# Performance work log

Hardware: AMD Instinct MI355X
Metric: run time of the kernel (lower is better)

The kernel has to match this reference:

```python
import jax, jax.numpy as jnp
import numpy as np

EMBD = 512
HEADS = 8
HEAD = EMBD // HEADS


def setup_inputs() -> dict:
    key = jax.random.key(0)
    ks = jax.random.split(key, 9)
    B, M = 4, 2048
    s = 1.0 / np.sqrt(EMBD)
    inp = {
        "x": jax.random.normal(ks[0], (B, M, EMBD), dtype=jnp.float32),
        "wq": jax.random.uniform(ks[1], (EMBD, EMBD), jnp.float32, -s, s),
        "bq": jnp.zeros((EMBD,), jnp.float32),
        "wk": jax.random.uniform(ks[2], (EMBD, EMBD), jnp.float32, -s, s),
        "bk": jnp.zeros((EMBD,), jnp.float32),
        "wv": jax.random.uniform(ks[3], (EMBD, EMBD), jnp.float32, -s, s),
        "bv": jnp.zeros((EMBD,), jnp.float32),
        "wo": jax.random.uniform(ks[4], (EMBD, EMBD), jnp.float32, -s, s),
        "bo": jnp.zeros((EMBD,), jnp.float32),
        "gamma": jnp.ones((EMBD,), jnp.float32),
        "beta": jnp.zeros((EMBD,), jnp.float32),
    }
    return inp


def layer_norm(x, gamma, beta, eps=1e-5):
    mu = jnp.mean(x, axis=-1, keepdims=True)
    var = jnp.mean(jnp.square(x - mu), axis=-1, keepdims=True)
    return (x - mu) * jax.lax.rsqrt(var + eps) * gamma + beta


def reference(x, wq, bq, wk, bk, wv, bv, wo, bo, gamma, beta):
    B, M, _ = x.shape
    norm = layer_norm(x, gamma, beta)
    # projections; reshape to [B, H, M, Dh]
    def proj(w, b):
        return (norm @ w.T + b).reshape(B, M, HEADS, HEAD).transpose(0, 2, 1, 3)
    q = proj(wq, bq)
    k = proj(wk, bk)
    v = proj(wv, bv)
    scores = jnp.einsum("bhmd,bhnd->bhmn", q, k) / np.sqrt(HEAD)
    # exclude self-attention on the diagonal
    diag = jnp.eye(M, dtype=bool)
    scores = jnp.where(diag, -jnp.inf, scores)
    attn = jax.nn.softmax(scores, axis=-1)
    ctx = jnp.einsum("bhmn,bhnd->bhmd", attn, v)
    ctx = ctx.transpose(0, 2, 1, 3).reshape(B, M, EMBD)
    out = ctx @ wo.T + bo
    return (out + x, attn)
```

## Files before the change

### kernel.cpp

```cpp
#include <hip/hip_runtime.h>

#define B_   4
#define H_   8
#define M_   2048
#define D_   512
#define DH_  64

typedef short  bf16x8 __attribute__((ext_vector_type(8)));
typedef short  bf16x4 __attribute__((ext_vector_type(4)));
typedef float  f32x4  __attribute__((ext_vector_type(4)));
typedef unsigned short u16x4 __attribute__((ext_vector_type(4)));
typedef unsigned int   u32x2 __attribute__((ext_vector_type(2)));

#define EXPC 0.18033688011112042f

static __device__ __forceinline__ unsigned short f2bf(float f) {
  unsigned u = __float_as_uint(f);
  u += 0x7fffu + ((u >> 16) & 1u);
  return (unsigned short)(u >> 16);
}

static __device__ __forceinline__ unsigned cvtpk(float lo, float hi) {
  unsigned r;
  asm("v_cvt_pk_bf16_f32 %0, %1, %2" : "=v"(r) : "v"(lo), "v"(hi));
  return r;
}

static __device__ __forceinline__ f32x4 mfma16(bf16x4 a, bf16x4 b, f32x4 c) {
  asm("v_mfma_f32_16x16x16_bf16 %0, %1, %2, %0" : "+v"(c) : "v"(a), "v"(b));
  return c;
}

static __device__ __forceinline__ int swz128(int row, int byteoff) {
  return row * 128 + (byteoff ^ ((row & 7) << 4));
}

static __device__ __forceinline__ void glds16(const void* g, void* l) {
  __builtin_amdgcn_global_load_lds(
      (const __attribute__((address_space(1))) unsigned*)g,
      (__attribute__((address_space(3))) unsigned*)l, 16, 0, 0);
}

static __device__ __forceinline__ void stage_tile(
    const char* g0, size_t rstride, char* lds, int t) {
  const int r0 = t >> 3, c0 = t & 7;
  const char* src = g0 + (size_t)r0 * rstride + ((c0 ^ (r0 & 7)) << 4);
  char* dst = lds + ((t & 192) << 4);
  #pragma unroll
  for (int c = 0; c < 4; ++c)
    glds16(src + (size_t)c * 32 * rstride, dst + c * 4096);
}

__global__ __launch_bounds__(256) void ln_kernel(
    const float* __restrict__ x, const float* __restrict__ gamma,
    const float* __restrict__ beta, unsigned short* __restrict__ xn)
{
  int row = blockIdx.x;
  int t = threadIdx.x;
  const float* xr = x + (size_t)row * D_;
  float v0 = xr[t], v1 = xr[t + 256];
  float s = v0 + v1, ss = v0 * v0 + v1 * v1;
  #pragma unroll
  for (int m = 1; m < 64; m <<= 1) {
    s  += __shfl_xor(s, m);
    ss += __shfl_xor(ss, m);
  }
  __shared__ float red[8];
  int wid = t >> 6;
  if ((t & 63) == 0) { red[wid] = s; red[wid + 4] = ss; }
  __syncthreads();
  s  = red[0] + red[1] + red[2] + red[3];
  ss = red[4] + red[5] + red[6] + red[7];
  float mu  = s * (1.0f / D_);
  float var = ss * (1.0f / D_) - mu * mu;
  float rstd = rsqrtf(var + 1e-5f);
  unsigned short* o = xn + (size_t)row * D_;
  o[t]       = f2bf((v0 - mu) * rstd * gamma[t]       + beta[t]);
  o[t + 256] = f2bf((v1 - mu) * rstd * gamma[t + 256] + beta[t + 256]);
}

__global__ __launch_bounds__(256) void cast_w_kernel(
    const float* __restrict__ wq, const float* __restrict__ wk,
    const float* __restrict__ wv, const float* __restrict__ wo,
    unsigned short* __restrict__ wqkv, unsigned short* __restrict__ wob)
{
  int i = blockIdx.x * 256 + threadIdx.x;
  wqkv[i]          = f2bf(wq[i]);
  wqkv[i + 262144] = f2bf(wk[i]);
  wqkv[i + 524288] = f2bf(wv[i]);
  wob[i]           = f2bf(wo[i]);
}

__global__ __launch_bounds__(256) void qkv_gemm(
    const unsigned short* __restrict__ xn,
    const unsigned short* __restrict__ wqkv,
    const float* __restrict__ bq, const float* __restrict__ bk,
    const float* __restrict__ bv,
    unsigned short* __restrict__ q, unsigned short* __restrict__ Kp,
    unsigned short* __restrict__ Vp)
{
  __shared__ __align__(16) char As[128 * 128];
  __shared__ __align__(16) char Bs[128 * 128];
  const int m0 = blockIdx.x * 128;
  const int n0 = blockIdx.y * 128;
  const int t = threadIdx.x, wid = t >> 6, lane = t & 63;
  const int wr = (wid >> 1) * 64, wc = (wid & 1) * 64;
  const int cl = lane & 15, rg = lane >> 4;
  const f32x4 z4 = {0.f, 0.f, 0.f, 0.f};
  const bool isv = (n0 >= 1024);

  const char* agb = (const char*)xn   + (size_t)m0 * 1024;
  const char* bgb = (const char*)wqkv + (size_t)n0 * 1024;

  f32x4 acc[4][4];
  #pragma unroll
  for (int i = 0; i < 4; ++i)
    #pragma unroll
    for (int j = 0; j < 4; ++j) acc[i][j] = z4;

  for (int k0 = 0; k0 < 512; k0 += 64) {
    __syncthreads();
    stage_tile(agb + k0 * 2, 1024, As, t);
    stage_tile(bgb + k0 * 2, 1024, Bs, t);
    __syncthreads();
    #pragma unroll
    for (int ks = 0; ks < 2; ++ks) {
      int koff = ks * 64 + rg * 16;
      bf16x8 af[4], bfr[4];
      #pragma unroll
      for (int i = 0; i < 4; ++i)
        af[i] = *(const bf16x8*)(As + swz128(wr + i * 16 + cl, koff));
      #pragma unroll
      for (int j = 0; j < 4; ++j)
        bfr[j] = *(const bf16x8*)(Bs + swz128(wc + j * 16 + cl, koff));
      if (isv) {
        #pragma unroll
        for (int i = 0; i < 4; ++i)
          #pragma unroll
          for (int j = 0; j < 4; ++j)
            acc[i][j] = __builtin_amdgcn_mfma_f32_16x16x32_bf16(af[i], bfr[j], acc[i][j], 0, 0, 0);
      } else {
        #pragma unroll
        for (int j = 0; j < 4; ++j)
          #pragma unroll
          for (int i = 0; i < 4; ++i)
            acc[j][i] = __builtin_amdgcn_mfma_f32_16x16x32_bf16(bfr[j], af[i], acc[j][i], 0, 0, 0);
      }
    }
  }

  if (isv) {
    #pragma unroll
    for (int j = 0; j < 4; ++j) {
      int n = n0 + wc + j * 16 + cl;
      int nn = n & 511;
      int h = nn >> 6, dh = nn & 63;
      int jd = dh >> 4, cld = dh & 15;
      float bias = bv[nn];
      #pragma unroll
      for (int i = 0; i < 4; ++i) {
        int mrow = m0 + wr + i * 16 + rg * 4;
        int b = mrow >> 11, mm = mrow & 2047;
        int nt = mm >> 6, nl = mm & 63;
        int jp = nl >> 5, half = (nl >> 4) & 1, rgv = (nl >> 2) & 3;
        u32x2 u;
        u[0] = cvtpk(acc[i][j][0] + bias, acc[i][j][1] + bias);
        u[1] = cvtpk(acc[i][j][2] + bias, acc[i][j][3] + bias);
        size_t off = ((((size_t)(b * H_ + h) * 32 + nt) * 4 + jd) * 2 + jp) * 512
                   + (rgv * 16 + cld) * 8 + half * 4;
        *(u16x4*)(Vp + off) = __builtin_bit_cast(u16x4, u);
      }
    }
  } else {
    const int mat = n0 >> 9;
    #pragma unroll
    for (int j = 0; j < 4; ++j) {
      int nn0 = ((n0 + wc) & 511) + j * 16 + rg * 4;
      int h = nn0 >> 6, dh = nn0 & 63;
      f32x4 b4 = *(const f32x4*)((mat ? bk : bq) + nn0);
      #pragma unroll
      for (int i = 0; i < 4; ++i) {
        int mrow = m0 + wr + i * 16 + cl;
        int b = mrow >> 11, mm = mrow & 2047;
        u32x2 u;
        u[0] = cvtpk(acc[j][i][0] + b4[0], acc[j][i][1] + b4[1]);
        u[1] = cvtpk(acc[j][i][2] + b4[2], acc[j][i][3] + b4[3]);
        if (mat == 0) {
          *(u16x4*)(q + ((size_t)(b * H_ + h) * M_ + mm) * DH_ + dh) =
              __builtin_bit_cast(u16x4, u);
        } else {
          int ks = dh >> 5, rgk = (dh >> 3) & 3, e0 = dh & 7;
          size_t off = ((((size_t)(b * H_ + h) * 32 + (mm >> 6)) * 4 + ((mm >> 4) & 3)) * 2 + ks) * 512
                     + (rgk * 16 + (mm & 15)) * 8 + e0;
          *(u16x4*)(Kp + off) = __builtin_bit_cast(u16x4, u);
        }
      }
    }
  }
}

__global__ __launch_bounds__(256, 4) void attn_kernel(
    const unsigned short* __restrict__ q,
    const unsigned short* __restrict__ Kp,
    const unsigned short* __restrict__ Vp,
    float* __restrict__ attn,
    unsigned short* __restrict__ ctx)
{
  __shared__ __align__(16) char Ps[4][2048];

  const int flat = blockIdx.x;
  const int bh = (flat & 7) * 4 + ((flat >> 3) >> 5);
  const int mb = (flat >> 3) & 31;
  const int m0 = mb * 64;
  const int t = threadIdx.x, wid = t >> 6, lane = t & 63;
  const int wr = wid * 16, cl = lane & 15, rg = lane >> 4;
  const int m_g = m0 + wr + cl;
  const f32x4 z4 = {0.f, 0.f, 0.f, 0.f};

  const char* qb = (const char*)(q + (size_t)bh * M_ * DH_);
  const unsigned short* kpb = Kp + (size_t)bh * 131072;
  const unsigned short* vpb = Vp + (size_t)bh * 131072;
  float* ab = attn + (size_t)bh * M_ * M_;

  bf16x8 qf[2];
  #pragma unroll
  for (int ks = 0; ks < 2; ++ks)
    qf[ks] = *(const bf16x8*)(qb + (size_t)m_g * 128 + ks * 64 + rg * 16);

  float psum = 0.f;
  for (int nt = 0; nt < 32; ++nt) {
    const unsigned short* kch = kpb + (size_t)nt * 4096;
    f32x4 s[4];
    #pragma unroll
    for (int j = 0; j < 4; ++j) s[j] = z4;
    #pragma unroll
    for (int ks = 0; ks < 2; ++ks)
      #pragma unroll
      for (int j = 0; j < 4; ++j) {
        bf16x8 kf = *(const bf16x8*)(kch + (j * 2 + ks) * 512 + lane * 8);
        s[j] = __builtin_amdgcn_mfma_f32_16x16x32_bf16(kf, qf[ks], s[j], 0, 0, 0);
      }
    if (nt == mb) {
      #pragma unroll
      for (int j = 0; j < 4; ++j)
        #pragma unroll
        for (int r = 0; r < 4; ++r) {
          int n_g = nt * 64 + j * 16 + rg * 4 + r;
          float p = __builtin_amdgcn_exp2f(s[j][r] * EXPC);
          psum += (n_g == m_g) ? 0.f : p;
        }
    } else {
      #pragma unroll
      for (int j = 0; j < 4; ++j)
        #pragma unroll
        for (int r = 0; r < 4; ++r)
          psum += __builtin_amdgcn_exp2f(s[j][r] * EXPC);
    }
  }
  psum += __shfl_xor(psum, 16);
  psum += __shfl_xor(psum, 32);
  const float rv = 1.0f / psum;

  f32x4 oc[4];
  #pragma unroll
  for (int j = 0; j < 4; ++j) oc[j] = z4;

  const int srow = lane >> 4;
  const int sch  = lane & 15;

  asm volatile("s_nop 7" :::);

  for (int nt = 0; nt < 32; ++nt) {
    const unsigned short* kch = kpb + (size_t)nt * 4096;
    const unsigned short* vch = vpb + (size_t)nt * 4096;
    f32x4 s[4];
    #pragma unroll
    for (int j = 0; j < 4; ++j) s[j] = z4;
    #pragma unroll
    for (int ks = 0; ks < 2; ++ks)
      #pragma unroll
      for (int j = 0; j < 4; ++j) {
        bf16x8 kf = *(const bf16x8*)(kch + (j * 2 + ks) * 512 + lane * 8);
        s[j] = __builtin_amdgcn_mfma_f32_16x16x32_bf16(kf, qf[ks], s[j], 0, 0, 0);
      }
    const bool dtile = (nt == mb);
    bf16x4 pb[4];
    #pragma unroll
    for (int j = 0; j < 4; ++j) {
      f32x4 pv;
      #pragma unroll
      for (int r = 0; r < 4; ++r) {
        int n_g = nt * 64 + j * 16 + rg * 4 + r;
        float p = __builtin_amdgcn_exp2f(s[j][r] * EXPC) * rv;
        pv[r] = (dtile && n_g == m_g) ? 0.f : p;
      }
      u32x2 u;
      u[0] = cvtpk(pv[0], pv[1]);
      u[1] = cvtpk(pv[2], pv[3]);
      pb[j] = __builtin_bit_cast(bf16x4, u);
      *(u32x2*)(Ps[wid] + swz128(cl, j * 32 + rg * 8)) = u;
    }
    {
      float* abase = ab + ((size_t)(m0 + wr + srow)) * M_ + nt * 64 + sch * 4;
      #pragma unroll
      for (int it = 0; it < 4; ++it) {
        u16x4 pu = *(const u16x4*)(Ps[wid] + swz128(it * 4 + srow, sch * 8));
        f32x4 pv;
        #pragma unroll
        for (int r = 0; r < 4; ++r) pv[r] = __uint_as_float((unsigned)pu[r] << 16);
        __builtin_nontemporal_store(pv, (f32x4*)(abase + (size_t)it * 4 * M_));
      }
    }
    #pragma unroll
    for (int jp = 0; jp < 2; ++jp)
      #pragma unroll
      for (int jd = 0; jd < 4; ++jd) {
        bf16x8 w = *(const bf16x8*)(vch + (jd * 2 + jp) * 512 + lane * 8);
        bf16x4 vlo = __builtin_shufflevector(w, w, 0, 1, 2, 3);
        bf16x4 vhi = __builtin_shufflevector(w, w, 4, 5, 6, 7);
        oc[jd] = mfma16(vlo, pb[jp * 2],     oc[jd]);
        oc[jd] = mfma16(vhi, pb[jp * 2 + 1], oc[jd]);
      }
  }

  asm volatile("s_nop 7\n\ts_nop 7" :::);

  int b = bh >> 3, h = bh & 7;
  unsigned short* crow = ctx + ((size_t)b * M_ + m_g) * D_ + h * DH_ + rg * 4;
  #pragma unroll
  for (int jd = 0; jd < 4; ++jd) {
    u32x2 u;
    u[0] = cvtpk(oc[jd][0], oc[jd][1]);
    u[1] = cvtpk(oc[jd][2], oc[jd][3]);
    *(u32x2*)(crow + jd * 16) = u;
  }
}

__global__ __launch_bounds__(256) void out_gemm(
    const unsigned short* __restrict__ ctxb,
    const unsigned short* __restrict__ wob,
    const float* __restrict__ bo,
    const float* __restrict__ x,
    float* __restrict__ out)
{
  __shared__ __align__(16) char As[128 * 128];
  __shared__ __align__(16) char Bs[128 * 128];
  const int m0 = blockIdx.x * 128;
  const int n0 = blockIdx.y * 128;
  const int t = threadIdx.x, wid = t >> 6, lane = t & 63;
  const int wr = (wid >> 1) * 64, wc = (wid & 1) * 64;
  const int cl = lane & 15, rg = lane >> 4;
  const f32x4 z4 = {0.f, 0.f, 0.f, 0.f};

  const char* agb = (const char*)ctxb + (size_t)m0 * 1024;
  const char* bgb = (const char*)wob  + (size_t)n0 * 1024;

  f32x4 acc[4][4];
  #pragma unroll
  for (int j = 0; j < 4; ++j)
    #pragma unroll
    for (int i = 0; i < 4; ++i) acc[j][i] = z4;

  for (int k0 = 0; k0 < 512; k0 += 64) {
    __syncthreads();
    stage_tile(agb + k0 * 2, 1024, As, t);
    stage_tile(bgb + k0 * 2, 1024, Bs, t);
    __syncthreads();
    #pragma unroll
    for (int ks = 0; ks < 2; ++ks) {
      int koff = ks * 64 + rg * 16;
      bf16x8 af[4], bfr[4];
      #pragma unroll
      for (int i = 0; i < 4; ++i)
        af[i] = *(const bf16x8*)(As + swz128(wr + i * 16 + cl, koff));
      #pragma unroll
      for (int j = 0; j < 4; ++j)
        bfr[j] = *(const bf16x8*)(Bs + swz128(wc + j * 16 + cl, koff));
      #pragma unroll
      for (int j = 0; j < 4; ++j)
        #pragma unroll
        for (int i = 0; i < 4; ++i)
          acc[j][i] = __builtin_amdgcn_mfma_f32_16x16x32_bf16(bfr[j], af[i], acc[j][i], 0, 0, 0);
    }
  }

  #pragma unroll
  for (int j = 0; j < 4; ++j) {
    int nb = n0 + wc + j * 16 + rg * 4;
    f32x4 bo4 = *(const f32x4*)(bo + nb);
    #pragma unroll
    for (int i = 0; i < 4; ++i) {
      int m = m0 + wr + i * 16 + cl;
      f32x4 x4 = *(const f32x4*)(x + (size_t)m * 512 + nb);
      f32x4 o;
      #pragma unroll
      for (int r = 0; r < 4; ++r) o[r] = acc[j][i][r] + bo4[r] + x4[r];
      *(f32x4*)(out + (size_t)m * 512 + nb) = o;
    }
  }
}

extern "C" void kernel_launch(void* const* d_in, const int* in_sizes, int n_in,
                              void* d_out, int out_size, void* d_ws, size_t ws_size,
                              hipStream_t stream) {
  const float* x     = (const float*)d_in[0];
  const float* wq    = (const float*)d_in[1];
  const float* bq    = (const float*)d_in[2];
  const float* wk    = (const float*)d_in[3];
  const float* bk    = (const float*)d_in[4];
  const float* wv    = (const float*)d_in[5];
  const float* bv    = (const float*)d_in[6];
  const float* wo    = (const float*)d_in[7];
  const float* bo    = (const float*)d_in[8];
  const float* gamma = (const float*)d_in[9];
  const float* beta  = (const float*)d_in[10];

  char* ws = (char*)d_ws;
  unsigned short* xn   = (unsigned short*)(ws);
  unsigned short* wqkv = (unsigned short*)(ws + 8388608);
  unsigned short* wob  = (unsigned short*)(ws + 9961472);
  unsigned short* qb   = (unsigned short*)(ws + 10485760);
  unsigned short* Kp   = (unsigned short*)(ws + 18874368);
  unsigned short* Vp   = (unsigned short*)(ws + 27262976);
  unsigned short* ctx  = (unsigned short*)(ws + 35651584);

  float* out  = (float*)d_out;
  float* attn = (float*)d_out + 4194304;

  ln_kernel<<<8192, 256, 0, stream>>>(x, gamma, beta, xn);
  cast_w_kernel<<<1024, 256, 0, stream>>>(wq, wk, wv, wo, wqkv, wob);
  qkv_gemm<<<dim3(64, 12), 256, 0, stream>>>(xn, wqkv, bq, bk, bv, qb, Kp, Vp);
  attn_kernel<<<1024, 256, 0, stream>>>(qb, Kp, Vp, attn, ctx);
  out_gemm<<<dim3(64, 4), 256, 0, stream>>>(ctx, wob, bo, x, out);
}
```

Measured before the change: 201.6 us.

## Process two query tiles per attention block and halve out-GEMM N tile

Each attention block now handles 128 query rows as two 64-row halves. The first half's output pass is fused with the second half's row-sum pass, so each K tile loaded from memory serves both halves. This cuts the number of K sweeps per query row from two to one and a half, at the cost of more registers and lower occupancy (launch bounds 2). The output GEMM switches to 128x64 tiles, doubling its grid to 512 blocks to fill more CUs.

```diff
diff --git a/kernel.cpp b/kernel.cpp
--- a/kernel.cpp
+++ b/kernel.cpp
@@ -49,6 +49,17 @@
   #pragma unroll
   for (int c = 0; c < 4; ++c)
     glds16(src + (size_t)c * 32 * rstride, dst + c * 4096);
+}
+
+static __device__ __forceinline__ void stage64(
+    const char* g0, size_t rstride, char* lds, int t) {
+  #pragma unroll
+  for (int c = 0; c < 2; ++c) {
+    int s = c * 256 + t;
+    int row = s >> 3, ch = s & 7;
+    const char* src = g0 + (size_t)row * rstride + ((ch ^ (row & 7)) << 4);
+    glds16(src, lds + c * 4096 + ((t & 192) << 4));
+  }
 }
 
 __global__ __launch_bounds__(256) void ln_kernel(
@@ -199,7 +210,7 @@
   }
 }
 
-__global__ __launch_bounds__(256, 4) void attn_kernel(
+__global__ __launch_bounds__(256, 2) void attn_kernel(
     const unsigned short* __restrict__ q,
     const unsigned short* __restrict__ Kp,
     const unsigned short* __restrict__ Vp,
@@ -209,12 +220,14 @@
   __shared__ __align__(16) char Ps[4][2048];
 
   const int flat = blockIdx.x;
-  const int bh = (flat & 7) * 4 + ((flat >> 3) >> 5);
-  const int mb = (flat >> 3) & 31;
-  const int m0 = mb * 64;
+  const int bh = (flat & 7) * 4 + ((flat >> 3) >> 4);
+  const int u  = (flat >> 3) & 15;
+  const int m0 = u * 128;
+  const int ntA = u * 2, ntB = u * 2 + 1;
   const int t = threadIdx.x, wid = t >> 6, lane = t & 63;
   const int wr = wid * 16, cl = lane & 15, rg = lane >> 4;
-  const int m_g = m0 + wr + cl;
+  const int mA = m0 + wr + cl;
+  const int mB = mA + 64;
   const f32x4 z4 = {0.f, 0.f, 0.f, 0.f};
 
   const char* qb = (const char*)(q + (size_t)bh * M_ * DH_);
@@ -222,12 +235,17 @@
   const unsigned short* vpb = Vp + (size_t)bh * 131072;
   float* ab = attn + (size_t)bh * M_ * M_;
 
-  bf16x8 qf[2];
-  #pragma unroll
-  for (int ks = 0; ks < 2; ++ks)
-    qf[ks] = *(const bf16x8*)(qb + (size_t)m_g * 128 + ks * 64 + rg * 16);
-
-  float psum = 0.f;
+  bf16x8 qfA[2], qfB[2];
+  #pragma unroll
+  for (int ks = 0; ks < 2; ++ks) {
+    qfA[ks] = *(const bf16x8*)(qb + (size_t)mA * 128 + ks * 64 + rg * 16);
+    qfB[ks] = *(const bf16x8*)(qb + (size_t)mB * 128 + ks * 64 + rg * 16);
+  }
+
+  const int srow = lane >> 4;
+  const int sch  = lane & 15;
+
+  float psumA = 0.f;
   for (int nt = 0; nt < 32; ++nt) {
     const unsigned short* kch = kpb + (size_t)nt * 4096;
     f32x4 s[4];
@@ -238,36 +256,136 @@
       #pragma unroll
       for (int j = 0; j < 4; ++j) {
         bf16x8 kf = *(const bf16x8*)(kch + (j * 2 + ks) * 512 + lane * 8);
-        s[j] = __builtin_amdgcn_mfma_f32_16x16x32_bf16(kf, qf[ks], s[j], 0, 0, 0);
-      }
-    if (nt == mb) {
+        s[j] = __builtin_amdgcn_mfma_f32_16x16x32_bf16(kf, qfA[ks], s[j], 0, 0, 0);
+      }
+    if (nt == ntA) {
       #pragma unroll
       for (int j = 0; j < 4; ++j)
         #pragma unroll
         for (int r = 0; r < 4; ++r) {
           int n_g = nt * 64 + j * 16 + rg * 4 + r;
           float p = __builtin_amdgcn_exp2f(s[j][r] * EXPC);
-          psum += (n_g == m_g) ? 0.f : p;
+          psumA += (n_g == mA) ? 0.f : p;
         }
     } else {
       #pragma unroll
       for (int j = 0; j < 4; ++j)
         #pragma unroll
         for (int r = 0; r < 4; ++r)
-          psum += __builtin_amdgcn_exp2f(s[j][r] * EXPC);
-    }
-  }
-  psum += __shfl_xor(psum, 16);
-  psum += __shfl_xor(psum, 32);
-  const float rv = 1.0f / psum;
-
-  f32x4 oc[4];
-  #pragma unroll
-  for (int j = 0; j < 4; ++j) oc[j] = z4;
-
-  const int srow = lane >> 4;
-  const int sch  = lane & 15;
-
+          psumA += __builtin_amdgcn_exp2f(s[j][r] * EXPC);
+    }
+  }
+  psumA += __shfl_xor(psumA, 16);
+  psumA += __shfl_xor(psumA, 32);
+  const float rvA = 1.0f / psumA;
+
+  asm volatile("s_nop 7" :::);
+
+  f32x4 ocA[4];
+  #pragma unroll
+  for (int j = 0; j < 4; ++j) ocA[j] = z4;
+  float psumB = 0.f;
+
+  for (int nt = 0; nt < 32; ++nt) {
+    const unsigned short* kch = kpb + (size_t)nt * 4096;
+    const unsigned short* vch = vpb + (size_t)nt * 4096;
+    bf16x8 kf[8], vf[8];
+    #pragma unroll
+    for (int jk = 0; jk < 8; ++jk)
+      kf[jk] = *(const bf16x8*)(kch + jk * 512 + lane * 8);
+    #pragma unroll
+    for (int jk = 0; jk < 8; ++jk)
+      vf[jk] = *(const bf16x8*)(vch + jk * 512 + lane * 8);
+    f32x4 s[4];
+    #pragma unroll
+    for (int j = 0; j < 4; ++j) s[j] = z4;
+    #pragma unroll
+    for (int ks = 0; ks < 2; ++ks)
+      #pragma unroll
+      for (int j = 0; j < 4; ++j)
+        s[j] = __builtin_amdgcn_mfma_f32_16x16x32_bf16(kf[j * 2 + ks], qfA[ks], s[j], 0, 0, 0);
+    const bool dA = (nt == ntA);
+    bf16x4 pb[4];
+    #pragma unroll
+    for (int j = 0; j < 4; ++j) {
+      f32x4 pv;
+      #pragma unroll
+      for (int r = 0; r < 4; ++r) {
+        int n_g = nt * 64 + j * 16 + rg * 4 + r;
+        float p = __builtin_amdgcn_exp2f(s[j][r] * EXPC) * rvA;
+        pv[r] = (dA && n_g == mA) ? 0.f : p;
+      }
+      u32x2 uu;
+      uu[0] = cvtpk(pv[0], pv[1]);
+      uu[1] = cvtpk(pv[2], pv[3]);
+      pb[j] = __builtin_bit_cast(bf16x4, uu);
+      *(u32x2*)(Ps[wid] + swz128(cl, j * 32 + rg * 8)) = uu;
+    }
+    {
+      float* abase = ab + ((size_t)(m0 + wr + srow)) * M_ + nt * 64 + sch * 4;
+      #pragma unroll
+      for (int it = 0; it < 4; ++it) {
+        u16x4 pu = *(const u16x4*)(Ps[wid] + swz128(it * 4 + srow, sch * 8));
+        f32x4 pv;
+        #pragma unroll
+        for (int r = 0; r < 4; ++r) pv[r] = __uint_as_float((unsigned)pu[r] << 16);
+        __builtin_nontemporal_store(pv, (f32x4*)(abase + (size_t)it * 4 * M_));
+      }
+    }
+    #pragma unroll
+    for (int jp = 0; jp < 2; ++jp)
+      #pragma unroll
+      for (int jd = 0; jd < 4; ++jd) {
+        bf16x8 w = vf[jd * 2 + jp];
+        bf16x4 vlo = __builtin_shufflevector(w, w, 0, 1, 2, 3);
+        bf16x4 vhi = __builtin_shufflevector(w, w, 4, 5, 6, 7);
+        ocA[jd] = mfma16(vlo, pb[jp * 2],     ocA[jd]);
+        ocA[jd] = mfma16(vhi, pb[jp * 2 + 1], ocA[jd]);
+      }
+    #pragma unroll
+    for (int j = 0; j < 4; ++j) s[j] = z4;
+    #pragma unroll
+    for (int ks = 0; ks < 2; ++ks)
+      #pragma unroll
+      for (int j = 0; j < 4; ++j)
+        s[j] = __builtin_amdgcn_mfma_f32_16x16x32_bf16(kf[j * 2 + ks], qfB[ks], s[j], 0, 0, 0);
+    if (nt == ntB) {
+      #pragma unroll
+      for (int j = 0; j < 4; ++j)
+        #pragma unroll
+        for (int r = 0; r < 4; ++r) {
+          int n_g = nt * 64 + j * 16 + rg * 4 + r;
+          float p = __builtin_amdgcn_exp2f(s[j][r] * EXPC);
+          psumB += (n_g == mB) ? 0.f : p;
+        }
+    } else {
+      #pragma unroll
+      for (int j = 0; j < 4; ++j)
+        #pragma unroll
+        for (int r = 0; r < 4; ++r)
+          psumB += __builtin_amdgcn_exp2f(s[j][r] * EXPC);
+    }
+  }
+  psumB += __shfl_xor(psumB, 16);
+  psumB += __shfl_xor(psumB, 32);
+  const float rvB = 1.0f / psumB;
+
+  {
+    int b = bh >> 3, h = bh & 7;
+    asm volatile("s_nop 7\n\ts_nop 7" :::);
+    unsigned short* crow = ctx + ((size_t)b * M_ + mA) * D_ + h * DH_ + rg * 4;
+    #pragma unroll
+    for (int jd = 0; jd < 4; ++jd) {
+      u32x2 uu;
+      uu[0] = cvtpk(ocA[jd][0], ocA[jd][1]);
+      uu[1] = cvtpk(ocA[jd][2], ocA[jd][3]);
+      *(u32x2*)(crow + jd * 16) = uu;
+    }
+  }
+
+  f32x4 ocB[4];
+  #pragma unroll
+  for (int j = 0; j < 4; ++j) ocB[j] = z4;
   asm volatile("s_nop 7" :::);
 
   for (int nt = 0; nt < 32; ++nt) {
@@ -281,9 +399,9 @@
       #pragma unroll
       for (int j = 0; j < 4; ++j) {
         bf16x8 kf = *(const bf16x8*)(kch + (j * 2 + ks) * 512 + lane * 8);
-        s[j] = __builtin_amdgcn_mfma_f32_16x16x32_bf16(kf, qf[ks], s[j], 0, 0, 0);
-      }
-    const bool dtile = (nt == mb);
+        s[j] = __builtin_amdgcn_mfma_f32_16x16x32_bf16(kf, qfB[ks], s[j], 0, 0, 0);
+      }
+    const bool dB = (nt == ntB);
     bf16x4 pb[4];
     #pragma unroll
     for (int j = 0; j < 4; ++j) {
@@ -291,17 +409,17 @@
       #pragma unroll
       for (int r = 0; r < 4; ++r) {
         int n_g = nt * 64 + j * 16 + rg * 4 + r;
-        float p = __builtin_amdgcn_exp2f(s[j][r] * EXPC) * rv;
-        pv[r] = (dtile && n_g == m_g) ? 0.f : p;
-      }
-      u32x2 u;
-      u[0] = cvtpk(pv[0], pv[1]);
-      u[1] = cvtpk(pv[2], pv[3]);
-      pb[j] = __builtin_bit_cast(bf16x4, u);
-      *(u32x2*)(Ps[wid] + swz128(cl, j * 32 + rg * 8)) = u;
+        float p = __builtin_amdgcn_exp2f(s[j][r] * EXPC) * rvB;
+        pv[r] = (dB && n_g == mB) ? 0.f : p;
+      }
+      u32x2 uu;
+      uu[0] = cvtpk(pv[0], pv[1]);
+      uu[1] = cvtpk(pv[2], pv[3]);
+      pb[j] = __builtin_bit_cast(bf16x4, uu);
+      *(u32x2*)(Ps[wid] + swz128(cl, j * 32 + rg * 8)) = uu;
     }
     {
-      float* abase = ab + ((size_t)(m0 + wr + srow)) * M_ + nt * 64 + sch * 4;
+      float* abase = ab + ((size_t)(m0 + 64 + wr + srow)) * M_ + nt * 64 + sch * 4;
       #pragma unroll
       for (int it = 0; it < 4; ++it) {
         u16x4 pu = *(const u16x4*)(Ps[wid] + swz128(it * 4 + srow, sch * 8));
@@ -318,21 +436,23 @@
         bf16x8 w = *(const bf16x8*)(vch + (jd * 2 + jp) * 512 + lane * 8);
         bf16x4 vlo = __builtin_shufflevector(w, w, 0, 1, 2, 3);
         bf16x4 vhi = __builtin_shufflevector(w, w, 4, 5, 6, 7);
-        oc[jd] = mfma16(vlo, pb[jp * 2],     oc[jd]);
-        oc[jd] = mfma16(vhi, pb[jp * 2 + 1], oc[jd]);
+        ocB[jd] = mfma16(vlo, pb[jp * 2],     ocB[jd]);
+        ocB[jd] = mfma16(vhi, pb[jp * 2 + 1], ocB[jd]);
       }
   }
 
   asm volatile("s_nop 7\n\ts_nop 7" :::);
 
-  int b = bh >> 3, h = bh & 7;
-  unsigned short* crow = ctx + ((size_t)b * M_ + m_g) * D_ + h * DH_ + rg * 4;
-  #pragma unroll
-  for (int jd = 0; jd < 4; ++jd) {
-    u32x2 u;
-    u[0] = cvtpk(oc[jd][0], oc[jd][1]);
-    u[1] = cvtpk(oc[jd][2], oc[jd][3]);
-    *(u32x2*)(crow + jd * 16) = u;
+  {
+    int b = bh >> 3, h = bh & 7;
+    unsigned short* crow = ctx + ((size_t)b * M_ + mB) * D_ + h * DH_ + rg * 4;
+    #pragma unroll
+    for (int jd = 0; jd < 4; ++jd) {
+      u32x2 uu;
+      uu[0] = cvtpk(ocB[jd][0], ocB[jd][1]);
+      uu[1] = cvtpk(ocB[jd][2], ocB[jd][3]);
+      *(u32x2*)(crow + jd * 16) = uu;
+    }
   }
 }
 
@@ -344,40 +464,40 @@
     float* __restrict__ out)
 {
   __shared__ __align__(16) char As[128 * 128];
-  __shared__ __align__(16) char Bs[128 * 128];
+  __shared__ __align__(16) char Bs[64 * 128];
   const int m0 = blockIdx.x * 128;
-  const int n0 = blockIdx.y * 128;
+  const int n0 = blockIdx.y * 64;
   const int t = threadIdx.x, wid = t >> 6, lane = t & 63;
-  const int wr = (wid >> 1) * 64, wc = (wid & 1) * 64;
+  const int wr = (wid >> 1) * 64, wc = (wid & 1) * 32;
   const int cl = lane & 15, rg = lane >> 4;
   const f32x4 z4 = {0.f, 0.f, 0.f, 0.f};
 
   const char* agb = (const char*)ctxb + (size_t)m0 * 1024;
   const char* bgb = (const char*)wob  + (size_t)n0 * 1024;
 
-  f32x4 acc[4][4];
-  #pragma unroll
-  for (int j = 0; j < 4; ++j)
+  f32x4 acc[2][4];
+  #pragma unroll
+  for (int j = 0; j < 2; ++j)
     #pragma unroll
     for (int i = 0; i < 4; ++i) acc[j][i] = z4;
 
   for (int k0 = 0; k0 < 512; k0 += 64) {
     __syncthreads();
     stage_tile(agb + k0 * 2, 1024, As, t);
-    stage_tile(bgb + k0 * 2, 1024, Bs, t);
+    stage64(bgb + k0 * 2, 1024, Bs, t);
     __syncthreads();
     #pragma unroll
     for (int ks = 0; ks < 2; ++ks) {
       int koff = ks * 64 + rg * 16;
-      bf16x8 af[4], bfr[4];
+      bf16x8 af[4], bfr[2];
       #pragma unroll
       for (int i = 0; i < 4; ++i)
         af[i] = *(const bf16x8*)(As + swz128(wr + i * 16 + cl, koff));
       #pragma unroll
-      for (int j = 0; j < 4; ++j)
+      for (int j = 0; j < 2; ++j)
         bfr[j] = *(const bf16x8*)(Bs + swz128(wc + j * 16 + cl, koff));
       #pragma unroll
-      for (int j = 0; j < 4; ++j)
+      for (int j = 0; j < 2; ++j)
         #pragma unroll
         for (int i = 0; i < 4; ++i)
           acc[j][i] = __builtin_amdgcn_mfma_f32_16x16x32_bf16(bfr[j], af[i], acc[j][i], 0, 0, 0);
@@ -385,7 +505,7 @@
   }
 
   #pragma unroll
-  for (int j = 0; j < 4; ++j) {
+  for (int j = 0; j < 2; ++j) {
     int nb = n0 + wc + j * 16 + rg * 4;
     f32x4 bo4 = *(const f32x4*)(bo + nb);
     #pragma unroll
@@ -430,6 +550,6 @@
   ln_kernel<<<8192, 256, 0, stream>>>(x, gamma, beta, xn);
   cast_w_kernel<<<1024, 256, 0, stream>>>(wq, wk, wv, wo, wqkv, wob);
   qkv_gemm<<<dim3(64, 12), 256, 0, stream>>>(xn, wqkv, bq, bk, bv, qb, Kp, Vp);
-  attn_kernel<<<1024, 256, 0, stream>>>(qb, Kp, Vp, attn, ctx);
-  out_gemm<<<dim3(64, 4), 256, 0, stream>>>(ctx, wob, bo, x, out);
-}
+  attn_kernel<<<512, 256, 0, stream>>>(qb, Kp, Vp, attn, ctx);
+  out_gemm<<<dim3(64, 8), 256, 0, stream>>>(ctx, wob, bo, x, out);
+}
```

New measurement: 199.0 us. Within noise of the previous version (-1.3%).

## Pipeline attention row-sum and output passes across warp groups; halve out_gemm N tile

Applied to the files above, without the earlier changes.

The attention kernel becomes 512-thread blocks, each owning four 64-row query tiles. One group of four waves computes the softmax row sums for tile s while the other group runs the normalized P·V and attention-matrix write for tile s-1, passing reciprocals through a double-buffered shared array and a block barrier. The aim is to overlap the store-heavy second pass with the compute-only first pass inside one block. Separately, out_gemm's N tile drops from 128 to 64 to double its grid. The cost is a barrier per stage, half the waves idle in the first and last stages, and fewer blocks for attention (256 instead of 1024).

```diff
diff --git a/kernel.cpp b/kernel.cpp
--- a/kernel.cpp
+++ b/kernel.cpp
@@ -49,6 +49,17 @@
   #pragma unroll
   for (int c = 0; c < 4; ++c)
     glds16(src + (size_t)c * 32 * rstride, dst + c * 4096);
+}
+
+static __device__ __forceinline__ void stage64(
+    const char* g0, size_t rstride, char* lds, int t) {
+  #pragma unroll
+  for (int c = 0; c < 2; ++c) {
+    int s = c * 256 + t;
+    int row = s >> 3, ch = s & 7;
+    const char* src = g0 + (size_t)row * rstride + ((ch ^ (row & 7)) << 4);
+    glds16(src, lds + c * 4096 + ((t & 192) << 4));
+  }
 }
 
 __global__ __launch_bounds__(256) void ln_kernel(
@@ -199,140 +210,151 @@
   }
 }
 
-__global__ __launch_bounds__(256, 4) void attn_kernel(
+__global__ __launch_bounds__(512, 4) void attn_kernel(
     const unsigned short* __restrict__ q,
     const unsigned short* __restrict__ Kp,
     const unsigned short* __restrict__ Vp,
     float* __restrict__ attn,
     unsigned short* __restrict__ ctx)
 {
-  __shared__ __align__(16) char Ps[4][2048];
-
-  const int flat = blockIdx.x;
-  const int bh = (flat & 7) * 4 + ((flat >> 3) >> 5);
-  const int mb = (flat >> 3) & 31;
-  const int m0 = mb * 64;
+  __shared__ __align__(16) char Ps[8][2048];
+  __shared__ float rvs[2][64];
+
+  const int bid = blockIdx.x;
+  const int bh   = (bid & 7) * 4 + (bid >> 6);
+  const int ublk = (bid >> 3) & 7;
+  const int u0   = ublk * 4;
   const int t = threadIdx.x, wid = t >> 6, lane = t & 63;
-  const int wr = wid * 16, cl = lane & 15, rg = lane >> 4;
-  const int m_g = m0 + wr + cl;
+  const int grp = wid >> 2, ws = wid & 3;
+  const int wr = ws * 16, cl = lane & 15, rg = lane >> 4;
   const f32x4 z4 = {0.f, 0.f, 0.f, 0.f};
 
   const char* qb = (const char*)(q + (size_t)bh * M_ * DH_);
   const unsigned short* kpb = Kp + (size_t)bh * 131072;
   const unsigned short* vpb = Vp + (size_t)bh * 131072;
   float* ab = attn + (size_t)bh * M_ * M_;
-
-  bf16x8 qf[2];
-  #pragma unroll
-  for (int ks = 0; ks < 2; ++ks)
-    qf[ks] = *(const bf16x8*)(qb + (size_t)m_g * 128 + ks * 64 + rg * 16);
-
-  float psum = 0.f;
-  for (int nt = 0; nt < 32; ++nt) {
-    const unsigned short* kch = kpb + (size_t)nt * 4096;
-    f32x4 s[4];
-    #pragma unroll
-    for (int j = 0; j < 4; ++j) s[j] = z4;
-    #pragma unroll
-    for (int ks = 0; ks < 2; ++ks)
-      #pragma unroll
-      for (int j = 0; j < 4; ++j) {
-        bf16x8 kf = *(const bf16x8*)(kch + (j * 2 + ks) * 512 + lane * 8);
-        s[j] = __builtin_amdgcn_mfma_f32_16x16x32_bf16(kf, qf[ks], s[j], 0, 0, 0);
-      }
-    if (nt == mb) {
-      #pragma unroll
-      for (int j = 0; j < 4; ++j)
-        #pragma unroll
-        for (int r = 0; r < 4; ++r) {
-          int n_g = nt * 64 + j * 16 + rg * 4 + r;
-          float p = __builtin_amdgcn_exp2f(s[j][r] * EXPC);
-          psum += (n_g == m_g) ? 0.f : p;
-        }
-    } else {
-      #pragma unroll
-      for (int j = 0; j < 4; ++j)
-        #pragma unroll
-        for (int r = 0; r < 4; ++r)
-          psum += __builtin_amdgcn_exp2f(s[j][r] * EXPC);
-    }
-  }
-  psum += __shfl_xor(psum, 16);
-  psum += __shfl_xor(psum, 32);
-  const float rv = 1.0f / psum;
-
-  f32x4 oc[4];
-  #pragma unroll
-  for (int j = 0; j < 4; ++j) oc[j] = z4;
+  const int b = bh >> 3, h = bh & 7;
 
   const int srow = lane >> 4;
   const int sch  = lane & 15;
 
-  asm volatile("s_nop 7" :::);
-
-  for (int nt = 0; nt < 32; ++nt) {
-    const unsigned short* kch = kpb + (size_t)nt * 4096;
-    const unsigned short* vch = vpb + (size_t)nt * 4096;
-    f32x4 s[4];
-    #pragma unroll
-    for (int j = 0; j < 4; ++j) s[j] = z4;
-    #pragma unroll
-    for (int ks = 0; ks < 2; ++ks)
-      #pragma unroll
-      for (int j = 0; j < 4; ++j) {
-        bf16x8 kf = *(const bf16x8*)(kch + (j * 2 + ks) * 512 + lane * 8);
-        s[j] = __builtin_amdgcn_mfma_f32_16x16x32_bf16(kf, qf[ks], s[j], 0, 0, 0);
-      }
-    const bool dtile = (nt == mb);
-    bf16x4 pb[4];
-    #pragma unroll
-    for (int j = 0; j < 4; ++j) {
-      f32x4 pv;
-      #pragma unroll
-      for (int r = 0; r < 4; ++r) {
-        int n_g = nt * 64 + j * 16 + rg * 4 + r;
-        float p = __builtin_amdgcn_exp2f(s[j][r] * EXPC) * rv;
-        pv[r] = (dtile && n_g == m_g) ? 0.f : p;
-      }
-      u32x2 u;
-      u[0] = cvtpk(pv[0], pv[1]);
-      u[1] = cvtpk(pv[2], pv[3]);
-      pb[j] = __builtin_bit_cast(bf16x4, u);
-      *(u32x2*)(Ps[wid] + swz128(cl, j * 32 + rg * 8)) = u;
-    }
-    {
-      float* abase = ab + ((size_t)(m0 + wr + srow)) * M_ + nt * 64 + sch * 4;
-      #pragma unroll
-      for (int it = 0; it < 4; ++it) {
-        u16x4 pu = *(const u16x4*)(Ps[wid] + swz128(it * 4 + srow, sch * 8));
-        f32x4 pv;
-        #pragma unroll
-        for (int r = 0; r < 4; ++r) pv[r] = __uint_as_float((unsigned)pu[r] << 16);
-        __builtin_nontemporal_store(pv, (f32x4*)(abase + (size_t)it * 4 * M_));
-      }
-    }
-    #pragma unroll
-    for (int jp = 0; jp < 2; ++jp)
+  for (int s = 0; s <= 4; ++s) {
+    if (grp == 0 && s < 4) {
+      const int u = u0 + s;
+      const int m_g = u * 64 + wr + cl;
+      bf16x8 qf[2];
+      #pragma unroll
+      for (int ks = 0; ks < 2; ++ks)
+        qf[ks] = *(const bf16x8*)(qb + (size_t)m_g * 128 + ks * 64 + rg * 16);
+      float psum = 0.f;
+      for (int nt = 0; nt < 32; ++nt) {
+        const unsigned short* kch = kpb + (size_t)nt * 4096;
+        f32x4 sj[4];
+        #pragma unroll
+        for (int j = 0; j < 4; ++j) sj[j] = z4;
+        #pragma unroll
+        for (int ks = 0; ks < 2; ++ks)
+          #pragma unroll
+          for (int j = 0; j < 4; ++j) {
+            bf16x8 kf = *(const bf16x8*)(kch + (j * 2 + ks) * 512 + lane * 8);
+            sj[j] = __builtin_amdgcn_mfma_f32_16x16x32_bf16(kf, qf[ks], sj[j], 0, 0, 0);
+          }
+        if (nt == u) {
+          #pragma unroll
+          for (int j = 0; j < 4; ++j)
+            #pragma unroll
+            for (int r = 0; r < 4; ++r) {
+              int n_g = nt * 64 + j * 16 + rg * 4 + r;
+              float p = __builtin_amdgcn_exp2f(sj[j][r] * EXPC);
+              psum += (n_g == m_g) ? 0.f : p;
+            }
+        } else {
+          #pragma unroll
+          for (int j = 0; j < 4; ++j)
+            #pragma unroll
+            for (int r = 0; r < 4; ++r)
+              psum += __builtin_amdgcn_exp2f(sj[j][r] * EXPC);
+        }
+      }
+      psum += __shfl_xor(psum, 16);
+      psum += __shfl_xor(psum, 32);
+      if (lane < 16) rvs[s & 1][wr + cl] = 1.0f / psum;
+    } else if (grp == 1 && s > 0) {
+      const int u = u0 + s - 1;
+      const int m_g = u * 64 + wr + cl;
+      const float rv = rvs[(s - 1) & 1][wr + cl];
+      bf16x8 qf[2];
+      #pragma unroll
+      for (int ks = 0; ks < 2; ++ks)
+        qf[ks] = *(const bf16x8*)(qb + (size_t)m_g * 128 + ks * 64 + rg * 16);
+      f32x4 oc[4];
+      #pragma unroll
+      for (int j = 0; j < 4; ++j) oc[j] = z4;
+      asm volatile("s_nop 7" :::);
+
+      for (int nt = 0; nt < 32; ++nt) {
+        const unsigned short* kch = kpb + (size_t)nt * 4096;
+        const unsigned short* vch = vpb + (size_t)nt * 4096;
+        f32x4 sj[4];
+        #pragma unroll
+        for (int j = 0; j < 4; ++j) sj[j] = z4;
+        #pragma unroll
+        for (int ks = 0; ks < 2; ++ks)
+          #pragma unroll
+          for (int j = 0; j < 4; ++j) {
+            bf16x8 kf = *(const bf16x8*)(kch + (j * 2 + ks) * 512 + lane * 8);
+            sj[j] = __builtin_amdgcn_mfma_f32_16x16x32_bf16(kf, qf[ks], sj[j], 0, 0, 0);
+          }
+        const bool dtile = (nt == u);
+        bf16x4 pb[4];
+        #pragma unroll
+        for (int j = 0; j < 4; ++j) {
+          f32x4 pv;
+          #pragma unroll
+          for (int r = 0; r < 4; ++r) {
+            int n_g = nt * 64 + j * 16 + rg * 4 + r;
+            float p = __builtin_amdgcn_exp2f(sj[j][r] * EXPC) * rv;
+            pv[r] = (dtile && n_g == m_g) ? 0.f : p;
+          }
+          u32x2 uu;
+          uu[0] = cvtpk(pv[0], pv[1]);
+          uu[1] = cvtpk(pv[2], pv[3]);
+          pb[j] = __builtin_bit_cast(bf16x4, uu);
+          *(u32x2*)(Ps[wid] + swz128(cl, j * 32 + rg * 8)) = uu;
+        }
+        {
+          float* abase = ab + ((size_t)(u * 64 + wr + srow)) * M_ + nt * 64 + sch * 4;
+          #pragma unroll
+          for (int it = 0; it < 4; ++it) {
+            u16x4 pu = *(const u16x4*)(Ps[wid] + swz128(it * 4 + srow, sch * 8));
+            f32x4 pv;
+            #pragma unroll
+            for (int r = 0; r < 4; ++r) pv[r] = __uint_as_float((unsigned)pu[r] << 16);
+            __builtin_nontemporal_store(pv, (f32x4*)(abase + (size_t)it * 4 * M_));
+          }
+        }
+        #pragma unroll
+        for (int jp = 0; jp < 2; ++jp)
+          #pragma unroll
+          for (int jd = 0; jd < 4; ++jd) {
+            bf16x8 w = *(const bf16x8*)(vch + (jd * 2 + jp) * 512 + lane * 8);
+            bf16x4 vlo = __builtin_shufflevector(w, w, 0, 1, 2, 3);
+            bf16x4 vhi = __builtin_shufflevector(w, w, 4, 5, 6, 7);
+            oc[jd] = mfma16(vlo, pb[jp * 2],     oc[jd]);
+            oc[jd] = mfma16(vhi, pb[jp * 2 + 1], oc[jd]);
+          }
+      }
+      asm volatile("s_nop 7\n\ts_nop 7" :::);
+      unsigned short* crow = ctx + ((size_t)b * M_ + m_g) * D_ + h * DH_ + rg * 4;
       #pragma unroll
       for (int jd = 0; jd < 4; ++jd) {
-        bf16x8 w = *(const bf16x8*)(vch + (jd * 2 + jp) * 512 + lane * 8);
-        bf16x4 vlo = __builtin_shufflevector(w, w, 0, 1, 2, 3);
-        bf16x4 vhi = __builtin_shufflevector(w, w, 4, 5, 6, 7);
-        oc[jd] = mfma16(vlo, pb[jp * 2],     oc[jd]);
-        oc[jd] = mfma16(vhi, pb[jp * 2 + 1], oc[jd]);
-      }
-  }
-
-  asm volatile("s_nop 7\n\ts_nop 7" :::);
-
-  int b = bh >> 3, h = bh & 7;
-  unsigned short* crow = ctx + ((size_t)b * M_ + m_g) * D_ + h * DH_ + rg * 4;
-  #pragma unroll
-  for (int jd = 0; jd < 4; ++jd) {
-    u32x2 u;
-    u[0] = cvtpk(oc[jd][0], oc[jd][1]);
-    u[1] = cvtpk(oc[jd][2], oc[jd][3]);
-    *(u32x2*)(crow + jd * 16) = u;
+        u32x2 uu;
+        uu[0] = cvtpk(oc[jd][0], oc[jd][1]);
+        uu[1] = cvtpk(oc[jd][2], oc[jd][3]);
+        *(u32x2*)(crow + jd * 16) = uu;
+      }
+    }
+    __syncthreads();
   }
 }
 
@@ -344,40 +366,40 @@
     float* __restrict__ out)
 {
   __shared__ __align__(16) char As[128 * 128];
-  __shared__ __align__(16) char Bs[128 * 128];
+  __shared__ __align__(16) char Bs[64 * 128];
   const int m0 = blockIdx.x * 128;
-  const int n0 = blockIdx.y * 128;
+  const int n0 = blockIdx.y * 64;
   const int t = threadIdx.x, wid = t >> 6, lane = t & 63;
-  const int wr = (wid >> 1) * 64, wc = (wid & 1) * 64;
+  const int wr = (wid >> 1) * 64, wc = (wid & 1) * 32;
   const int cl = lane & 15, rg = lane >> 4;
   const f32x4 z4 = {0.f, 0.f, 0.f, 0.f};
 
   const char* agb = (const char*)ctxb + (size_t)m0 * 1024;
   const char* bgb = (const char*)wob  + (size_t)n0 * 1024;
 
-  f32x4 acc[4][4];
-  #pragma unroll
-  for (int j = 0; j < 4; ++j)
+  f32x4 acc[2][4];
+  #pragma unroll
+  for (int j = 0; j < 2; ++j)
     #pragma unroll
     for (int i = 0; i < 4; ++i) acc[j][i] = z4;
 
   for (int k0 = 0; k0 < 512; k0 += 64) {
     __syncthreads();
     stage_tile(agb + k0 * 2, 1024, As, t);
-    stage_tile(bgb + k0 * 2, 1024, Bs, t);
+    stage64(bgb + k0 * 2, 1024, Bs, t);
     __syncthreads();
     #pragma unroll
     for (int ks = 0; ks < 2; ++ks) {
       int koff = ks * 64 + rg * 16;
-      bf16x8 af[4], bfr[4];
+      bf16x8 af[4], bfr[2];
       #pragma unroll
       for (int i = 0; i < 4; ++i)
         af[i] = *(const bf16x8*)(As + swz128(wr + i * 16 + cl, koff));
       #pragma unroll
-      for (int j = 0; j < 4; ++j)
+      for (int j = 0; j < 2; ++j)
         bfr[j] = *(const bf16x8*)(Bs + swz128(wc + j * 16 + cl, koff));
       #pragma unroll
-      for (int j = 0; j < 4; ++j)
+      for (int j = 0; j < 2; ++j)
         #pragma unroll
         for (int i = 0; i < 4; ++i)
           acc[j][i] = __builtin_amdgcn_mfma_f32_16x16x32_bf16(bfr[j], af[i], acc[j][i], 0, 0, 0);
@@ -385,7 +407,7 @@
   }
 
   #pragma unroll
-  for (int j = 0; j < 4; ++j) {
+  for (int j = 0; j < 2; ++j) {
     int nb = n0 + wc + j * 16 + rg * 4;
     f32x4 bo4 = *(const f32x4*)(bo + nb);
     #pragma unroll
@@ -430,6 +452,6 @@
   ln_kernel<<<8192, 256, 0, stream>>>(x, gamma, beta, xn);
   cast_w_kernel<<<1024, 256, 0, stream>>>(wq, wk, wv, wo, wqkv, wob);
   qkv_gemm<<<dim3(64, 12), 256, 0, stream>>>(xn, wqkv, bq, bk, bv, qb, Kp, Vp);
-  attn_kernel<<<1024, 256, 0, stream>>>(qb, Kp, Vp, attn, ctx);
-  out_gemm<<<dim3(64, 4), 256, 0, stream>>>(ctx, wob, bo, x, out);
-}
+  attn_kernel<<<256, 512, 0, stream>>>(qb, Kp, Vp, attn, ctx);
+  out_gemm<<<dim3(64, 8), 256, 0, stream>>>(ctx, wob, bo, x, out);
+}
```

Result: no change. 198.3 us (-1.6%).
